# Kernel tuning notes

Hardware: AMD Instinct MI355X
Metric: run time of the kernel (lower is better)

## Reference

```python
import jax, jax.numpy as jnp
import numpy as np

D_MODEL = 1024
NUM_HEADS = 16
HEAD_DIM = D_MODEL // NUM_HEADS
B, S = 2, 2048


def setup_inputs() -> dict:
    key = jax.random.key(0)
    ks = jax.random.split(key, 10)
    sc = 1.0 / np.sqrt(D_MODEL)
    return {
        "x": jax.random.normal(ks[0], (B, S, D_MODEL), jnp.float32),
        "y": jax.random.normal(ks[1], (B, S, D_MODEL), jnp.float32),
        "Wkv": jax.random.normal(ks[2], (D_MODEL, 2 * D_MODEL), jnp.float32) * sc,
        "bkv": jax.random.normal(ks[3], (2 * D_MODEL,), jnp.float32) * 0.01,
        "Wq": jax.random.normal(ks[4], (D_MODEL, D_MODEL), jnp.float32) * sc,
        "bq": jax.random.normal(ks[5], (D_MODEL,), jnp.float32) * 0.01,
        "Wo": jax.random.normal(ks[6], (D_MODEL, D_MODEL), jnp.float32) * sc,
        "bo": jax.random.normal(ks[7], (D_MODEL,), jnp.float32) * 0.01,
    }


def reference(x, y, Wkv, bkv, Wq, bq, Wo, bo):
    b, s, d = x.shape
    # projections: kv from x (keys/values come from encoder side), q from y
    kv = x @ Wkv + bkv                      # [B, S, 2*d_model]
    q = y @ Wq + bq                         # [B, S, d_model]
    kv = kv.reshape(b, s, NUM_HEADS, 2 * HEAD_DIM).transpose(0, 2, 1, 3)  # [B,H,S,2*hd]
    q = q.reshape(b, s, NUM_HEADS, HEAD_DIM).transpose(0, 2, 1, 3)        # [B,H,S,hd]
    k, v = jnp.split(kv, 2, axis=-1)        # each [B,H,S,hd]
    scaled = jnp.einsum("bhqd,bhkd->bhqk", q, k) / np.sqrt(HEAD_DIM)      # [B,H,S,S]
    attention = jax.nn.softmax(scaled, axis=-1)
    values = jnp.einsum("bhqk,bhkd->bhqd", attention, v)                  # [B,H,S,hd]
    values = values.transpose(0, 2, 1, 3).reshape(b, s, d)                # [B,S,d_model]
    return values @ Wo + bo
```

## Files before the change

### kernel.cpp

```cpp
#include <hip/hip_runtime.h>
#include <hip/hip_bf16.h>

typedef __attribute__((ext_vector_type(8))) short short8;
typedef __attribute__((ext_vector_type(4))) short short4v;
typedef __attribute__((ext_vector_type(4))) float f32x4;

#define B_  2
#define S_  2048
#define H_  16
#define HD_ 64
#define D_  1024
#define QSCALE 0.18033688f

__device__ __forceinline__ short f2bs(float f) {
  union { float f; unsigned u; } c; c.f = f;
  unsigned u = c.u;
  u += 0x7fffu + ((u >> 16) & 1u);
  return (short)(u >> 16);
}

__device__ __forceinline__ unsigned pack_bf16(float a, float b) {
  __hip_bfloat162 h = __float22bfloat162_rn(float2{a, b});
  return *reinterpret_cast<unsigned*>(&h);
}

__device__ __forceinline__ float fexp2(float x) {
#if __has_builtin(__builtin_amdgcn_exp2f)
  return __builtin_amdgcn_exp2f(x);
#else
  return exp2f(x);
#endif
}

__device__ __forceinline__ float frcp(float x) {
#if __has_builtin(__builtin_amdgcn_rcpf)
  return __builtin_amdgcn_rcpf(x);
#else
  return 1.0f / x;
#endif
}

#define GL2LDS(gp, lp) __builtin_amdgcn_global_load_lds( \
    (const __attribute__((address_space(1))) unsigned int*)(gp), \
    (__attribute__((address_space(3))) unsigned int*)(lp), 16, 0, 0)

__global__ __launch_bounds__(256)
void prep_kernel(const float* __restrict__ x, const float* __restrict__ y,
                 short* __restrict__ xb, short* __restrict__ yb,
                 const float* __restrict__ Wkv, short* __restrict__ Wkvt,
                 const float* __restrict__ Wq, short* __restrict__ Wqt,
                 const float* __restrict__ Wo, short* __restrict__ Wot) {
  __shared__ float tile[64][65];
  int bx = blockIdx.x;
  if (bx < 8192) {
    int i = bx * 256 + threadIdx.x;
    const float4* src; short4v* dst; int j;
    if (i < (1 << 20)) { src = (const float4*)x; dst = (short4v*)xb; j = i; }
    else               { src = (const float4*)y; dst = (short4v*)yb; j = i - (1 << 20); }
    float4 f = src[j];
    short4v o;
    o.x = f2bs(f.x); o.y = f2bs(f.y); o.z = f2bs(f.z); o.w = f2bs(f.w);
    dst[j] = o;
    return;
  }
  bx -= 8192;
  const float* in; short* out; int C, c0, r0;
  if (bx < 512)      { in = Wkv; out = Wkvt; C = 2048; c0 = (bx & 31) * 64; r0 = (bx >> 5) * 64; }
  else if (bx < 768) { bx -= 512; in = Wq; out = Wqt; C = 1024; c0 = (bx & 15) * 64; r0 = (bx >> 4) * 64; }
  else               { bx -= 768; in = Wo; out = Wot; C = 1024; c0 = (bx & 15) * 64; r0 = (bx >> 4) * 64; }
  const int tx = threadIdx.x & 63, ty = threadIdx.x >> 6;
#pragma unroll
  for (int i = 0; i < 16; ++i) {
    int r = ty + i * 4;
    tile[r][tx] = in[(size_t)(r0 + r) * C + c0 + tx];
  }
  __syncthreads();
#pragma unroll
  for (int i = 0; i < 16; ++i) {
    int r = ty + i * 4;
    out[(size_t)(c0 + r) * 1024 + r0 + tx] = f2bs(tile[tx][r]);
  }
}

template <int MODE>
__device__ __forceinline__ void gemm_body(const short* __restrict__ A, const short* __restrict__ Bt,
                                          const float* __restrict__ bias,
                                          void* __restrict__ out0, void* __restrict__ out1,
                                          int m0, int n0, int K, short* smem) {
  short* As = smem;
  short* Bs = smem + 4096;
  const int tid = threadIdx.x;
  const int w = tid >> 6, lane = tid & 63;
  const int q15 = lane & 15, quad = lane >> 4;
  const int wm = (w >> 1) * 64, wn = (w & 1) * 64;

  f32x4 acc[4][4];
#pragma unroll
  for (int i = 0; i < 4; ++i)
#pragma unroll
    for (int j = 0; j < 4; ++j) acc[i][j] = f32x4{0.f, 0.f, 0.f, 0.f};

  const int srow = w * 16 + (lane >> 2);
  const int gch  = (lane & 3) ^ ((lane >> 3) & 3);
  const short* Ag = A + (size_t)(m0 + srow) * K + gch * 8;
  const short* Bg = Bt + (size_t)(n0 + srow) * K + gch * 8;
  short* Al = As + srow * 32 + (lane & 3) * 8;
  short* Bl = Bs + srow * 32 + (lane & 3) * 8;

  for (int kt = 0; kt < K; kt += 32) {
    GL2LDS(Ag + kt,                  Al);
    GL2LDS(Ag + kt + (size_t)64 * K, Al + 64 * 32);
    GL2LDS(Bg + kt,                  Bl);
    GL2LDS(Bg + kt + (size_t)64 * K, Bl + 64 * 32);
    __syncthreads();
    short8 af[4], bf[4];
#pragma unroll
    for (int mi = 0; mi < 4; ++mi) {
      int rr = wm + mi * 16 + q15;
      af[mi] = *(const short8*)(As + rr * 32 + ((quad ^ ((rr >> 1) & 3)) * 8));
    }
#pragma unroll
    for (int ni = 0; ni < 4; ++ni) {
      int rr = wn + ni * 16 + q15;
      bf[ni] = *(const short8*)(Bs + rr * 32 + ((quad ^ ((rr >> 1) & 3)) * 8));
    }
#pragma unroll
    for (int mi = 0; mi < 4; ++mi)
#pragma unroll
      for (int ni = 0; ni < 4; ++ni)
        acc[mi][ni] = __builtin_amdgcn_mfma_f32_16x16x32_bf16(af[mi], bf[ni], acc[mi][ni], 0, 0, 0);
    __syncthreads();
  }

  if constexpr (MODE == 0) {
#pragma unroll
    for (int mi = 0; mi < 4; ++mi)
#pragma unroll
      for (int ni = 0; ni < 4; ++ni) {
        const int n = n0 + wn + ni * 16 + q15;
        const float bn = bias[n];
#pragma unroll
        for (int r = 0; r < 4; ++r) {
          const int m = m0 + wm + mi * 16 + quad * 4 + r;
          int b = m >> 11, s = m & 2047, hh = n >> 6, d = n & 63;
          ((short*)out0)[((size_t)((b * H_ + hh) * S_ + s) << 6) + d] = f2bs((acc[mi][ni][r] + bn) * QSCALE);
        }
      }
  } else {
    const int hh = n0 >> 7;
    const int bb = m0 >> 11;
    const size_t bh = (size_t)(bb * H_ + hh);
    const int s0 = m0 & 2047;
    if ((w & 1) == 0) {
#pragma unroll
      for (int mi = 0; mi < 4; ++mi)
#pragma unroll
        for (int ni = 0; ni < 4; ++ni) {
          const float bn = bias[n0 + ni * 16 + q15];
#pragma unroll
          for (int r = 0; r < 4; ++r) {
            const int s = s0 + wm + mi * 16 + quad * 4 + r;
            ((short*)out0)[((bh * S_ + s) << 6) + ni * 16 + q15] = f2bs(acc[mi][ni][r] + bn);
          }
        }
    } else {
      short* VT = smem;
#pragma unroll
      for (int mi = 0; mi < 4; ++mi)
#pragma unroll
        for (int ni = 0; ni < 4; ++ni) {
          const int d = ni * 16 + q15;
          const float bn = bias[n0 + 64 + ni * 16 + q15];
#pragma unroll
          for (int t = 0; t < 2; ++t) {
            const int chunk = (wm >> 1) + mi * 8 + quad * 2 + t;
            unsigned pk = pack_bf16(acc[mi][ni][2 * t] + bn, acc[mi][ni][2 * t + 1] + bn);
            *reinterpret_cast<unsigned*>(VT + d * 128 + ((chunk ^ (d & 15)) * 2)) = pk;
          }
        }
    }
    __syncthreads();
    {
      short* VT = smem;
      const int d = tid >> 2, t4 = tid & 3;
      unsigned vals[16];
#pragma unroll
      for (int c = 0; c < 16; ++c) {
        int chunk = t4 * 16 + c;
        vals[c] = *reinterpret_cast<unsigned*>(VT + d * 128 + ((chunk ^ (d & 15)) * 2));
      }
      uint4* dst = (uint4*)((short*)out1 + ((bh * HD_ + d) << 11) + s0 + t4 * 32);
      dst[0] = uint4{vals[0], vals[1], vals[2], vals[3]};
      dst[1] = uint4{vals[4], vals[5], vals[6], vals[7]};
      dst[2] = uint4{vals[8], vals[9], vals[10], vals[11]};
      dst[3] = uint4{vals[12], vals[13], vals[14], vals[15]};
    }
  }
}

__global__ __launch_bounds__(256)
void proj_kernel(const short* __restrict__ xb, const short* __restrict__ Wkvt,
                 const float* __restrict__ bkv, short* __restrict__ Kb, short* __restrict__ Vtb,
                 const short* __restrict__ yb, const short* __restrict__ Wqt,
                 const float* __restrict__ bq, short* __restrict__ Qb) {
  __shared__ __align__(16) short smem[8192];
  int bx = blockIdx.x;
  if (bx < 512)
    gemm_body<1>(xb, Wkvt, bkv, Kb, Vtb, (bx >> 4) * 128, (bx & 15) * 128, 1024, smem);
  else {
    bx -= 512;
    gemm_body<0>(yb, Wqt, bq, Qb, nullptr, (bx >> 3) * 128, (bx & 7) * 128, 1024, smem);
  }
}

__global__ __launch_bounds__(256)
void gemm_o_kernel(const short* __restrict__ A, const short* __restrict__ Bt,
                   const float* __restrict__ bias, float* __restrict__ out) {
  __shared__ __align__(16) short lds[16384];
  const int tid = threadIdx.x;
  const int w = tid >> 6, lane = tid & 63;
  const int q15 = lane & 15, quad = lane >> 4;
  const int m0 = blockIdx.y * 64, n0 = blockIdx.x * 64;
  const int wm = (w >> 1) * 32, wn = (w & 1) * 32;
  const int xw = q15 & 7;

  f32x4 acc[2][2];
#pragma unroll
  for (int i = 0; i < 2; ++i)
#pragma unroll
    for (int j = 0; j < 2; ++j) acc[i][j] = f32x4{0.f, 0.f, 0.f, 0.f};

  const int srow = w * 8 + (lane >> 3);
  const int gch  = (lane & 7) ^ (srow & 7);
  const int loff = w * 512 + lane * 8;
  const short* Ag = A + (size_t)(m0 + srow) * 1024 + gch * 8;
  const short* Bg = Bt + (size_t)(n0 + srow) * 1024 + gch * 8;

  GL2LDS(Ag,             lds + loff);
  GL2LDS(Ag + 32 * 1024, lds + loff + 2048);
  GL2LDS(Bg,             lds + 8192 + loff);
  GL2LDS(Bg + 32 * 1024, lds + 8192 + loff + 2048);

  for (int kt = 0; kt < 16; ++kt) {
    __syncthreads();
    const short* Ac = lds + ((kt & 1) ? 4096 : 0);
    const short* Bc = lds + 8192 + ((kt & 1) ? 4096 : 0);
    if (kt < 15) {
      const short* a2 = Ag + (kt + 1) * 64;
      const short* b2 = Bg + (kt + 1) * 64;
      short* ad = lds + ((kt & 1) ? 0 : 4096) + loff;
      short* bd = lds + 8192 + ((kt & 1) ? 0 : 4096) + loff;
      GL2LDS(a2,             ad);
      GL2LDS(a2 + 32 * 1024, ad + 2048);
      GL2LDS(b2,             bd);
      GL2LDS(b2 + 32 * 1024, bd + 2048);
    }
    short8 af[2][2], bf[2][2];
#pragma unroll
    for (int mi = 0; mi < 2; ++mi)
#pragma unroll
      for (int kk = 0; kk < 2; ++kk)
        af[mi][kk] = *(const short8*)(Ac + (wm + mi * 16 + q15) * 64 + (((kk * 4 + quad) ^ xw) * 8));
#pragma unroll
    for (int ni = 0; ni < 2; ++ni)
#pragma unroll
      for (int kk = 0; kk < 2; ++kk)
        bf[ni][kk] = *(const short8*)(Bc + (wn + ni * 16 + q15) * 64 + (((kk * 4 + quad) ^ xw) * 8));
#pragma unroll
    for (int mi = 0; mi < 2; ++mi)
#pragma unroll
      for (int ni = 0; ni < 2; ++ni)
#pragma unroll
        for (int kk = 0; kk < 2; ++kk)
          acc[mi][ni] = __builtin_amdgcn_mfma_f32_16x16x32_bf16(af[mi][kk], bf[ni][kk], acc[mi][ni], 0, 0, 0);
  }

#pragma unroll
  for (int mi = 0; mi < 2; ++mi)
#pragma unroll
    for (int ni = 0; ni < 2; ++ni) {
      const int n = n0 + wn + ni * 16 + q15;
      const float bn = bias[n];
#pragma unroll
      for (int r = 0; r < 4; ++r) {
        const int m = m0 + wm + mi * 16 + quad * 4 + r;
        out[(size_t)m * 1024 + n] = acc[mi][ni][r] + bn;
      }
    }
}

__global__ __launch_bounds__(512, 2)
void attn_kernel(const short* __restrict__ Q, const short* __restrict__ K,
                 const short* __restrict__ Vt, short* __restrict__ Out) {
  __shared__ __align__(16) short lds[32768];
  short* QP = lds + 16384;
  const int tid = threadIdx.x;
  const int w = tid >> 6, lane = tid & 63;
  const int q15 = lane & 15, quad = lane >> 4;
  const int xw = q15 & 7;
  const int bx = blockIdx.x;
  const int xcd = bx & 7, slot = bx >> 3;
  const int pp = xcd * 4 + (slot >> 3);
  const int qt = slot & 7;
  const int h = pp & 15, b = pp >> 4;
  const size_t bh = (size_t)(b * H_ + h);
  const short* Qg = Q + bh * (S_ * HD_) + qt * (256 * HD_);
  const short* Kg = K + bh * (S_ * HD_);
  const short* Vg = Vt + bh * (HD_ * S_);

  const int srow = w * 8 + (lane >> 3);
  const int gch  = (lane & 7) ^ (srow & 7);
  const int loff = w * 512 + lane * 8;

  {
    const short* qg = Qg + srow * 64 + gch * 8;
#pragma unroll
    for (int t = 0; t < 4; ++t) GL2LDS(qg + t * 4096, QP + loff + t * 4096);
  }
  const short* kg = Kg + srow * 64 + gch * 8;
  const short* vg = Vg + (size_t)srow * S_ + gch * 8;
  GL2LDS(kg, lds + loff);
  GL2LDS(vg, lds + 8192 + loff);
  __syncthreads();

  short8 aq[2][2];
#pragma unroll
  for (int st = 0; st < 2; ++st)
#pragma unroll
    for (int kk = 0; kk < 2; ++kk)
      aq[st][kk] = *(const short8*)(QP + (w * 32 + st * 16 + q15) * 64 + (((kk * 4 + quad) ^ xw) * 8));
  short* Pb[2] = { QP + w * 2048, QP + w * 2048 + 1024 };

  f32x4 oacc[2][4];
#pragma unroll
  for (int st = 0; st < 2; ++st)
#pragma unroll
    for (int ni = 0; ni < 4; ++ni) oacc[st][ni] = f32x4{0.f, 0.f, 0.f, 0.f};
  float lsum[2] = {0.f, 0.f};
  const f32x4 zz = {0.f, 0.f, 0.f, 0.f};

  for (int kt = 0; kt < 32; ++kt) {
    __syncthreads();
    const short* Kc = lds + ((kt & 1) ? 4096 : 0);
    const short* Vc = lds + 8192 + ((kt & 1) ? 4096 : 0);
    if (kt < 31) {
      const short* k2 = kg + (kt + 1) * 4096;
      const short* v2 = vg + (kt + 1) * 64;
      GL2LDS(k2, lds + ((kt & 1) ? 0 : 4096) + loff);
      GL2LDS(v2, lds + 8192 + ((kt & 1) ? 0 : 4096) + loff);
    }

    f32x4 sacc[2][4];
#pragma unroll
    for (int mi = 0; mi < 4; ++mi) {
      const short* kr = Kc + (mi * 16 + q15) * 64;
      short8 a0 = *(const short8*)(kr + ((quad ^ xw) * 8));
      short8 a1 = *(const short8*)(kr + (((quad + 4) ^ xw) * 8));
#pragma unroll
      for (int st = 0; st < 2; ++st) {
        f32x4 t = __builtin_amdgcn_mfma_f32_16x16x32_bf16(a0, aq[st][0], zz, 0, 0, 0);
        sacc[st][mi] = __builtin_amdgcn_mfma_f32_16x16x32_bf16(a1, aq[st][1], t, 0, 0, 0);
      }
    }

#pragma unroll
    for (int st = 0; st < 2; ++st)
#pragma unroll
      for (int mi = 0; mi < 4; ++mi) {
        float p0 = fexp2(sacc[st][mi][0]), p1 = fexp2(sacc[st][mi][1]);
        float p2 = fexp2(sacc[st][mi][2]), p3 = fexp2(sacc[st][mi][3]);
        lsum[st] += (p0 + p1) + (p2 + p3);
        uint2 pk;
        pk.x = pack_bf16(p0, p1);
        pk.y = pack_bf16(p2, p3);
        *reinterpret_cast<uint2*>(Pb[st] + q15 * 64 +
                                  (((mi * 2 + (quad >> 1)) ^ xw) * 8) + (quad & 1) * 4) = pk;
      }

    short8 ap[2][2];
#pragma unroll
    for (int st = 0; st < 2; ++st)
#pragma unroll
      for (int kk = 0; kk < 2; ++kk)
        ap[st][kk] = *(const short8*)(Pb[st] + q15 * 64 + (((kk * 4 + quad) ^ xw) * 8));
#pragma unroll
    for (int ni = 0; ni < 4; ++ni) {
      const short* vr = Vc + (ni * 16 + q15) * 64;
#pragma unroll
      for (int kk = 0; kk < 2; ++kk) {
        short8 bv = *(const short8*)(vr + (((kk * 4 + quad) ^ xw) * 8));
#pragma unroll
        for (int st = 0; st < 2; ++st)
          oacc[st][ni] = __builtin_amdgcn_mfma_f32_16x16x32_bf16(ap[st][kk], bv, oacc[st][ni], 0, 0, 0);
      }
    }
  }

#pragma unroll
  for (int st = 0; st < 2; ++st) {
    float l = lsum[st];
    l += __shfl_xor(l, 16);
    l += __shfl_xor(l, 32);
    float inv[4];
#pragma unroll
    for (int r = 0; r < 4; ++r) inv[r] = frcp(__shfl(l, quad * 4 + r, 64));
#pragma unroll
    for (int ni = 0; ni < 4; ++ni) {
      const int col = h * HD_ + ni * 16 + q15;
#pragma unroll
      for (int r = 0; r < 4; ++r) {
        const int m = b * S_ + qt * 256 + w * 32 + st * 16 + quad * 4 + r;
        Out[(size_t)m * D_ + col] = f2bs(oacc[st][ni][r] * inv[r]);
      }
    }
  }
}

extern "C" void kernel_launch(void* const* d_in, const int* in_sizes, int n_in,
                              void* d_out, int out_size, void* d_ws, size_t ws_size,
                              hipStream_t stream) {
  const float* x   = (const float*)d_in[0];
  const float* y   = (const float*)d_in[1];
  const float* Wkv = (const float*)d_in[2];
  const float* bkv = (const float*)d_in[3];
  const float* Wq  = (const float*)d_in[4];
  const float* bq  = (const float*)d_in[5];
  const float* Wo  = (const float*)d_in[6];
  const float* bo  = (const float*)d_in[7];
  float* out = (float*)d_out;

  short* xb   = (short*)d_ws;
  short* yb   = xb + (4 << 20);
  short* Wkvt = yb + (4 << 20);
  short* Wqt  = Wkvt + (2 << 20);
  short* Wot  = Wqt + (1 << 20);
  short* Kb   = Wot + (1 << 20);
  short* Vtb  = Kb + (4 << 20);
  short* Qb   = Vtb + (4 << 20);
  short* AOb  = Qb + (4 << 20);

  prep_kernel<<<9216, 256, 0, stream>>>(x, y, xb, yb, Wkv, Wkvt, Wq, Wqt, Wo, Wot);
  proj_kernel<<<768, 256, 0, stream>>>(xb, Wkvt, bkv, Kb, Vtb, yb, Wqt, bq, Qb);
  attn_kernel<<<256, 512, 0, stream>>>(Qb, Kb, Vtb, AOb);
  gemm_o_kernel<<<dim3(16, 64), 256, 0, stream>>>(AOb, Wot, bo, out);
}
```

Measured before the change: 209.0 us.

## Double-buffer projection GEMM LDS tiles and remap blocks for XCD locality

The projection GEMM now keeps two LDS tiles. It prefetches the next K-slice into the spare buffer while the current one feeds the MFMAs, which drops one barrier per iteration and hides global-load latency. It also permutes the block index so blocks dispatched round-robin across XCDs work on neighbouring output tiles, aiming for better L2 reuse. LDS use per block doubles, which may reduce occupancy.

```diff
diff --git a/kernel.cpp b/kernel.cpp
--- a/kernel.cpp
+++ b/kernel.cpp
@@ -87,8 +87,8 @@
                                           const float* __restrict__ bias,
                                           void* __restrict__ out0, void* __restrict__ out1,
                                           int m0, int n0, int K, short* smem) {
-  short* As = smem;
-  short* Bs = smem + 4096;
+  short* As_ = smem;
+  short* Bs_ = smem + 8192;
   const int tid = threadIdx.x;
   const int w = tid >> 6, lane = tid & 63;
   const int q15 = lane & 15, quad = lane >> 4;
@@ -104,33 +104,46 @@
   const int gch  = (lane & 3) ^ ((lane >> 3) & 3);
   const short* Ag = A + (size_t)(m0 + srow) * K + gch * 8;
   const short* Bg = Bt + (size_t)(n0 + srow) * K + gch * 8;
-  short* Al = As + srow * 32 + (lane & 3) * 8;
-  short* Bl = Bs + srow * 32 + (lane & 3) * 8;
-
-  for (int kt = 0; kt < K; kt += 32) {
-    GL2LDS(Ag + kt,                  Al);
-    GL2LDS(Ag + kt + (size_t)64 * K, Al + 64 * 32);
-    GL2LDS(Bg + kt,                  Bl);
-    GL2LDS(Bg + kt + (size_t)64 * K, Bl + 64 * 32);
+  const int lof = srow * 32 + (lane & 3) * 8;
+
+  GL2LDS(Ag,                  As_ + lof);
+  GL2LDS(Ag + (size_t)64 * K, As_ + lof + 2048);
+  GL2LDS(Bg,                  Bs_ + lof);
+  GL2LDS(Bg + (size_t)64 * K, Bs_ + lof + 2048);
+
+  const int NT = K >> 5;
+  for (int kt = 0; kt < NT; ++kt) {
     __syncthreads();
+    const short* Ac = As_ + (kt & 1) * 4096;
+    const short* Bc = Bs_ + (kt & 1) * 4096;
+    if (kt + 1 < NT) {
+      const short* a2 = Ag + (size_t)(kt + 1) * 32;
+      const short* b2 = Bg + (size_t)(kt + 1) * 32;
+      short* ad = As_ + ((kt & 1) ^ 1) * 4096 + lof;
+      short* bd = Bs_ + ((kt & 1) ^ 1) * 4096 + lof;
+      GL2LDS(a2,                  ad);
+      GL2LDS(a2 + (size_t)64 * K, ad + 2048);
+      GL2LDS(b2,                  bd);
+      GL2LDS(b2 + (size_t)64 * K, bd + 2048);
+    }
     short8 af[4], bf[4];
 #pragma unroll
     for (int mi = 0; mi < 4; ++mi) {
       int rr = wm + mi * 16 + q15;
-      af[mi] = *(const short8*)(As + rr * 32 + ((quad ^ ((rr >> 1) & 3)) * 8));
+      af[mi] = *(const short8*)(Ac + rr * 32 + ((quad ^ ((rr >> 1) & 3)) * 8));
     }
 #pragma unroll
     for (int ni = 0; ni < 4; ++ni) {
       int rr = wn + ni * 16 + q15;
-      bf[ni] = *(const short8*)(Bs + rr * 32 + ((quad ^ ((rr >> 1) & 3)) * 8));
+      bf[ni] = *(const short8*)(Bc + rr * 32 + ((quad ^ ((rr >> 1) & 3)) * 8));
     }
 #pragma unroll
     for (int mi = 0; mi < 4; ++mi)
 #pragma unroll
       for (int ni = 0; ni < 4; ++ni)
         acc[mi][ni] = __builtin_amdgcn_mfma_f32_16x16x32_bf16(af[mi], bf[ni], acc[mi][ni], 0, 0, 0);
-    __syncthreads();
-  }
+  }
+  __syncthreads();
 
   if constexpr (MODE == 0) {
 #pragma unroll
@@ -203,8 +216,9 @@
                  const float* __restrict__ bkv, short* __restrict__ Kb, short* __restrict__ Vtb,
                  const short* __restrict__ yb, const short* __restrict__ Wqt,
                  const float* __restrict__ bq, short* __restrict__ Qb) {
-  __shared__ __align__(16) short smem[8192];
+  __shared__ __align__(16) short smem[16384];
   int bx = blockIdx.x;
+  bx = (bx & 7) * 96 + (bx >> 3);
   if (bx < 512)
     gemm_body<1>(xb, Wkvt, bkv, Kb, Vtb, (bx >> 4) * 128, (bx & 15) * 128, 1024, smem);
   else {
```

Result: faster. 204.6 us (-2.1%).
